# Kernel optimization log

Measured on AMD Instinct MI355X. Metric: run time of the kernel, lower is better.

The kernel has to match this reference:

```python
import jax, jax.numpy as jnp
import numpy as np

MAX_SPAN = 16
EPS = 1e-12


def setup_inputs() -> dict:
    key = jax.random.key(0)
    ks = jax.random.split(key, 10)
    B, S, H, R = 64, 512, 768, 51
    embed = jax.random.normal(ks[0], (B, S, H), dtype=jnp.float32)
    sub_head = jax.random.randint(ks[1], (B,), 0, S - MAX_SPAN, dtype=jnp.int32)
    span = jax.random.randint(ks[2], (B,), 0, MAX_SPAN, dtype=jnp.int32)
    sub_tail = sub_head + span  # guaranteed valid span inside [0, S)
    s = 0.02
    W_ih = jax.random.normal(ks[3], (4 * H, H), dtype=jnp.float32) * s
    W_hh = jax.random.normal(ks[4], (4 * H, H), dtype=jnp.float32) * s
    b_ih = jnp.zeros((4 * H,), dtype=jnp.float32)
    b_hh = jnp.zeros((4 * H,), dtype=jnp.float32)
    cln_weight = jnp.ones((H,), dtype=jnp.float32)
    cln_bias = jnp.zeros((H,), dtype=jnp.float32)
    # nonzero so the conditional path is exercised (init is zeros in torch)
    cln_Ww = jax.random.normal(ks[5], (H, H), dtype=jnp.float32) * s
    cln_Wb = jax.random.normal(ks[6], (H, H), dtype=jnp.float32) * s
    Wh = jax.random.normal(ks[7], (R, H), dtype=jnp.float32) * s
    bh = jnp.zeros((R,), dtype=jnp.float32)
    Wt = jax.random.normal(ks[8], (R, H), dtype=jnp.float32) * s
    bt = jnp.zeros((R,), dtype=jnp.float32)
    return {"embed": embed, "sub_head": sub_head, "sub_tail": sub_tail,
            "W_ih": W_ih, "W_hh": W_hh, "b_ih": b_ih, "b_hh": b_hh,
            "cln_weight": cln_weight, "cln_bias": cln_bias,
            "cln_Ww": cln_Ww, "cln_Wb": cln_Wb,
            "Wh": Wh, "bh": bh, "Wt": Wt, "bt": bt}


def _ragged_lstm(embed, sub_head, sub_tail, W_ih, W_hh, b_ih, b_hh):
    # Pack ragged spans [head, tail] into a padded [B, MAX_SPAN, H] block and
    # run one batched LSTM scan, freezing state once past each span's end.
    B, S, H = embed.shape
    offs = jnp.arange(MAX_SPAN, dtype=sub_head.dtype)
    pos = sub_head[:, None] + offs[None, :]                    # [B, T]
    idx = jnp.clip(pos, 0, S - 1)
    x = jnp.take_along_axis(embed, idx[:, :, None], axis=1)    # [B, T, H]
    mask = pos <= sub_tail[:, None]                            # [B, T]

    def step(carry, inp):
        h, c = carry
        xt, mt = inp                                           # [B,H], [B]
        gates = xt @ W_ih.T + b_ih + h @ W_hh.T + b_hh         # [B, 4H]
        i, f, g, o = jnp.split(gates, 4, axis=-1)
        c_new = jax.nn.sigmoid(f) * c + jax.nn.sigmoid(i) * jnp.tanh(g)
        h_new = jax.nn.sigmoid(o) * jnp.tanh(c_new)
        m = mt[:, None]
        h = jnp.where(m, h_new, h)
        c = jnp.where(m, c_new, c)
        return (h, c), None

    h0 = jnp.zeros((B, H), dtype=embed.dtype)
    (hn, _), _ = jax.lax.scan(step, (h0, h0),
                              (x.transpose(1, 0, 2), mask.T))
    return hn                                                  # [B, H]


def _cond_layernorm(inputs, cond, weight, bias, Ww, Wb):
    # weight/bias are conditioned on `cond` via zero-init dense layers
    w = cond @ Ww.T + weight                                   # [B, H]
    b = cond @ Wb.T + bias
    mu = jnp.mean(inputs, axis=-1, keepdims=True)
    xc = inputs - mu
    var = jnp.mean(xc * xc, axis=-1, keepdims=True)
    std = jnp.sqrt(var + EPS)
    return w[:, None, :] * xc / (std + EPS) + b[:, None, :]


def reference(embed, sub_head, sub_tail, W_ih, W_hh, b_ih, b_hh,
              cln_weight, cln_bias, cln_Ww, cln_Wb, Wh, bh, Wt, bt):
    sub_embed = _ragged_lstm(embed, sub_head, sub_tail, W_ih, W_hh, b_ih, b_hh)
    new_embed = _cond_layernorm(embed, sub_embed, cln_weight, cln_bias,
                                cln_Ww, cln_Wb)
    heads = jax.nn.sigmoid(new_embed @ Wh.T + bh)              # [B, S, R]
    tails = jax.nn.sigmoid(new_embed @ Wt.T + bt)
    return heads, tails
```

## Files before the change

kernel.cpp:

```cpp
#include <hip/hip_runtime.h>

typedef __attribute__((ext_vector_type(8))) short bhalf8;
typedef __attribute__((ext_vector_type(4))) float floatx4;


__device__ unsigned short g_whh[3072*768];
__device__ unsigned short g_wih[3072*768];
__device__ unsigned short g_wcln[1536*768];
__device__ unsigned short g_whl[128*768];
__device__ unsigned short g_h2[2*64*768];
__device__ float g_cbuf[64*768];
__device__ float g_xg[1024*3072];
__device__ float g_wv[64*768], g_bv[64*768];
__device__ float g_bias[3072];
__device__ float g_cw[768], g_cb[768];
__device__ float g_bh[64], g_bt[64];

static __device__ __forceinline__ unsigned short f2bf(float f){
  unsigned u = __builtin_bit_cast(unsigned, f);
  u = (u + 0x7FFFu + ((u >> 16) & 1u)) >> 16;
  return (unsigned short)u;
}
static __device__ __forceinline__ float sigm(float x){ return 1.0f/(1.0f + __expf(-x)); }
static __device__ __forceinline__ float tanhq(float x){ float e = __expf(-2.0f*x); return (1.0f - e)/(1.0f + e); }

__global__ __launch_bounds__(256) void casrel_prep(
    const float* __restrict__ W_ih, const float* __restrict__ W_hh,
    const float* __restrict__ Ww,   const float* __restrict__ Wb,
    const float* __restrict__ Wh,   const float* __restrict__ Wt,
    const float* __restrict__ b_ih, const float* __restrict__ b_hh,
    const float* __restrict__ cw,   const float* __restrict__ cb,
    const float* __restrict__ bh,   const float* __restrict__ bt){
  const long NW = 2359296, NC = 1179648, NL = 98304;
  const long NH = 98304, NCF = 49152, NB = 3072, NV = 768, NR = 64;
  const long total = NW*2 + NC + NL + NH + NCF + NB + NV*2 + NR*2;
  for(long i = (long)blockIdx.x*256 + threadIdx.x; i < total; i += (long)gridDim.x*256){
    long j = i;
    if(j < NW){ g_whh[j] = f2bf(W_hh[j]); continue; } j -= NW;
    if(j < NW){ g_wih[j] = f2bf(W_ih[j]); continue; } j -= NW;
    if(j < NC){ g_wcln[j] = (j < 589824) ? f2bf(Ww[j]) : f2bf(Wb[j - 589824]); continue; } j -= NC;
    if(j < NL){ long r = j / 768, k = j - r*768;
                float v = 0.0f;
                if(r < 51) v = Wh[r*768 + k]; else if(r < 102) v = Wt[(r-51)*768 + k];
                g_whl[j] = f2bf(v); continue; } j -= NL;
    if(j < NH){ g_h2[j] = 0; continue; } j -= NH;
    if(j < NCF){ g_cbuf[j] = 0.0f; continue; } j -= NCF;
    if(j < NB){ g_bias[j] = b_ih[j] + b_hh[j]; continue; } j -= NB;
    if(j < NV){ g_cw[j] = cw[j]; continue; } j -= NV;
    if(j < NV){ g_cb[j] = cb[j]; continue; } j -= NV;
    if(j < NR){ g_bh[j] = (j < 51) ? bh[j] : 0.0f; continue; } j -= NR;
    g_bt[j] = (j < 51) ? bt[j] : 0.0f;
  }
}

__global__ __launch_bounds__(256) void casrel_xgates(
    const float* __restrict__ embed, const int* __restrict__ head){
  __shared__ char sB[128*128];
  const int tid = threadIdx.x, l = tid & 63, w = tid >> 6;
  const int n0 = blockIdx.x * 128;
  const int m0 = blockIdx.y * 64 + w*16;
  const int mrow = m0 + (l & 15);
  const int b = mrow >> 4, t = mrow & 15;
  int pos = head[b] + t; pos = pos < 0 ? 0 : (pos > 511 ? 511 : pos);
  const float* aptr = embed + ((long)b*512 + pos)*768 + ((l >> 4)*8);
  floatx4 acc[8];
  #pragma unroll
  for(int q=0;q<8;q++){ acc[q][0]=0.f; acc[q][1]=0.f; acc[q][2]=0.f; acc[q][3]=0.f; }
  for(int kt=0; kt<12; ++kt){
    __syncthreads();
    #pragma unroll
    for(int j=0;j<4;j++){
      int f = tid + 256*j;
      int row = f >> 3, seg = f & 7;
      uint4 v = *(const uint4*)(g_wih + ((long)(n0+row))*768 + kt*64 + seg*8);
      *(uint4*)(sB + row*128 + ((seg*16) ^ ((row & 7) << 4))) = v;
    }
    __syncthreads();
    #pragma unroll
    for(int ks=0; ks<2; ++ks){
      const int k = kt*64 + ks*32;
      float4 lo = *(const float4*)(aptr + k);
      float4 hi = *(const float4*)(aptr + k + 4);
      bhalf8 a;
      a[0]=(short)f2bf(lo.x); a[1]=(short)f2bf(lo.y); a[2]=(short)f2bf(lo.z); a[3]=(short)f2bf(lo.w);
      a[4]=(short)f2bf(hi.x); a[5]=(short)f2bf(hi.y); a[6]=(short)f2bf(hi.z); a[7]=(short)f2bf(hi.w);
      const int kb = ks*64 + ((l >> 4)*16);
      #pragma unroll
      for(int q=0;q<8;q++){
        int row = q*16 + (l & 15);
        bhalf8 bb = *(const bhalf8*)(sB + row*128 + (kb ^ ((row & 7) << 4)));
        acc[q] = __builtin_amdgcn_mfma_f32_16x16x32_bf16(a, bb, acc[q], 0, 0, 0);
      }
    }
  }
  #pragma unroll
  for(int q=0;q<8;q++){
    const int n = n0 + q*16 + (l & 15);
    const float bias = g_bias[n];
    #pragma unroll
    for(int r=0;r<4;r++){
      const int m = m0 + (l >> 4)*4 + r;
      g_xg[(long)m*3072 + n] = acc[q][r] + bias;
    }
  }
}

__global__ __launch_bounds__(256) void casrel_step(
    const int* __restrict__ head, const int* __restrict__ tail, int t){
  __shared__ char sW[64*768];
  const unsigned short* hin = g_h2 + (t & 1)*49152;
  unsigned short* hout = g_h2 + ((t & 1) ^ 1)*49152;
  const int tid = threadIdx.x, l = tid & 63, w = tid >> 6;
  const int j0 = blockIdx.x * 16;
  const int jown = j0 + (l & 15);
  const int arow = w*16 + (l & 15);
  floatx4 acc[4];
  #pragma unroll
  for(int g=0;g<4;g++){ acc[g][0]=0.f; acc[g][1]=0.f; acc[g][2]=0.f; acc[g][3]=0.f; }
  for(int kt=0; kt<2; ++kt){
    __syncthreads();
    #pragma unroll
    for(int j=0;j<12;j++){
      int f = tid + 256*j;
      int row = f / 48, seg = f - row*48;
      int grow = (row >> 4)*768 + j0 + (row & 15);
      uint4 v = *(const uint4*)(g_whh + (long)grow*768 + kt*384 + seg*8);
      *(uint4*)(sW + row*768 + ((seg*16) ^ ((row & 7) << 4))) = v;
    }
    __syncthreads();
    const unsigned short* ap = hin + arow*768 + kt*384 + ((l >> 4)*8);
    #pragma unroll 4
    for(int ks=0; ks<12; ++ks){
      bhalf8 a = *(const bhalf8*)(ap + ks*32);
      const int kb = ks*64 + ((l >> 4)*16);
      #pragma unroll
      for(int g=0;g<4;g++){
        int row = g*16 + (l & 15);
        bhalf8 bb = *(const bhalf8*)(sW + row*768 + (kb ^ ((row & 7) << 4)));
        acc[g] = __builtin_amdgcn_mfma_f32_16x16x32_bf16(a, bb, acc[g], 0, 0, 0);
      }
    }
  }
  #pragma unroll
  for(int r=0;r<4;r++){
    const int b = w*16 + (l >> 4)*4 + r;
    const int cell = b*768 + jown;
    const float* xp = g_xg + ((long)(b*16 + t))*3072 + jown;
    float Gi = acc[0][r] + xp[0];
    float Gf = acc[1][r] + xp[768];
    float Gg = acc[2][r] + xp[1536];
    float Go = acc[3][r] + xp[2304];
    if(t <= tail[b] - head[b]){
      float c = g_cbuf[cell];
      float ig = sigm(Gi), fg = sigm(Gf), gg = tanhq(Gg), og = sigm(Go);
      c = fg*c + ig*gg;
      g_cbuf[cell] = c;
      hout[cell] = f2bf(og*tanhq(c));
    } else {
      hout[cell] = hin[cell];
    }
  }
}

__global__ __launch_bounds__(256) void casrel_clnproj(){
  __shared__ char sW[32*1536];
  const int tid = threadIdx.x, l = tid & 63, w = tid >> 6;
  const int n0c = blockIdx.x * 32;
  #pragma unroll
  for(int j=0;j<12;j++){
    int f = tid + 256*j;
    int row = f / 96, seg = f - row*96;
    uint4 v = *(const uint4*)(g_wcln + (long)(n0c+row)*768 + seg*8);
    *(uint4*)(sW + row*1536 + ((seg*16) ^ ((row & 7) << 4))) = v;
  }
  __syncthreads();
  const int arow = w*16 + (l & 15);
  floatx4 acc2[2];
  #pragma unroll
  for(int q=0;q<2;q++){ acc2[q][0]=0.f; acc2[q][1]=0.f; acc2[q][2]=0.f; acc2[q][3]=0.f; }
  const unsigned short* ap2 = g_h2 + arow*768 + ((l >> 4)*8);
  for(int ks=0; ks<24; ++ks){
    bhalf8 a = *(const bhalf8*)(ap2 + ks*32);
    const int kb = ks*64 + ((l >> 4)*16);
    #pragma unroll
    for(int q=0;q<2;q++){
      int row = q*16 + (l & 15);
      bhalf8 bb = *(const bhalf8*)(sW + row*1536 + (kb ^ ((row & 7) << 4)));
      acc2[q] = __builtin_amdgcn_mfma_f32_16x16x32_bf16(a, bb, acc2[q], 0, 0, 0);
    }
  }
  #pragma unroll
  for(int q=0;q<2;q++){
    const int n = n0c + q*16 + (l & 15);
    #pragma unroll
    for(int r=0;r<4;r++){
      const int b = w*16 + (l >> 4)*4 + r;
      float v = acc2[q][r];
      if(n < 768) g_wv[b*768 + n] = v + g_cw[n];
      else        g_bv[b*768 + (n - 768)] = v + g_cb[n - 768];
    }
  }
}

__global__ __launch_bounds__(256) void casrel_out(
    const float* __restrict__ embed, float* __restrict__ out){
  __shared__ char sB[128*128];
  __shared__ char sE[32*128];
  __shared__ float sMu[32], sRs[32];
  const int tid = threadIdx.x, l = tid & 63, w = tid >> 6;
  const int b = blockIdx.y;
  const int s0 = blockIdx.x * 32;
  const float* xbase = embed + ((long)b*512 + s0)*768;
  for(int rr=0; rr<8; ++rr){
    const int row = w*8 + rr;
    const float* rp = xbase + row*768;
    float sm = 0.f, sq = 0.f;
    #pragma unroll
    for(int q=0;q<3;q++){
      float4 v = *(const float4*)(rp + l*4 + q*256);
      sm += v.x + v.y + v.z + v.w;
      sq += v.x*v.x + v.y*v.y + v.z*v.z + v.w*v.w;
    }
    #pragma unroll
    for(int o=32;o>0;o>>=1){ sm += __shfl_xor(sm, o); sq += __shfl_xor(sq, o); }
    if(l == 0){
      float mu = sm * (1.0f/768.0f);
      float var = sq * (1.0f/768.0f) - mu*mu;
      sMu[row] = mu;
      sRs[row] = 1.0f/(sqrtf(var + 1e-12f) + 1e-12f);
    }
  }
  __syncthreads();
  const int mf = w >> 1, nb = (w & 1)*4;
  floatx4 acc[4];
  #pragma unroll
  for(int q=0;q<4;q++){ acc[q][0]=0.f; acc[q][1]=0.f; acc[q][2]=0.f; acc[q][3]=0.f; }
  for(int kt=0; kt<12; ++kt){
    __syncthreads();
    #pragma unroll
    for(int j=0;j<4;j++){
      int f = tid + 256*j;
      int row = f >> 3, seg = f & 7;
      uint4 v = *(const uint4*)(g_whl + (long)row*768 + kt*64 + seg*8);
      *(uint4*)(sB + row*128 + ((seg*16) ^ ((row & 7) << 4))) = v;
    }
    #pragma unroll
    for(int j=0;j<2;j++){
      int f = tid + 256*j;
      int row = f >> 4, cs = f & 15;
      int k = kt*64 + cs*4;
      float4 x4 = *(const float4*)(xbase + row*768 + k);
      float4 w4 = *(const float4*)(g_wv + b*768 + k);
      float4 c4 = *(const float4*)(g_bv + b*768 + k);
      float mu = sMu[row], rs = sRs[row];
      unsigned long long pk =
          (unsigned long long)f2bf((x4.x - mu)*rs*w4.x + c4.x)
        | ((unsigned long long)f2bf((x4.y - mu)*rs*w4.y + c4.y) << 16)
        | ((unsigned long long)f2bf((x4.z - mu)*rs*w4.z + c4.z) << 32)
        | ((unsigned long long)f2bf((x4.w - mu)*rs*w4.w + c4.w) << 48);
      *(unsigned long long*)(sE + row*128 + ((cs*8) ^ ((row & 7) << 4))) = pk;
    }
    __syncthreads();
    #pragma unroll
    for(int ks=0; ks<2; ++ks){
      const int arow = mf*16 + (l & 15);
      const int kb = ks*64 + ((l >> 4)*16);
      bhalf8 a = *(const bhalf8*)(sE + arow*128 + (kb ^ ((arow & 7) << 4)));
      #pragma unroll
      for(int q=0;q<4;q++){
        int row = (nb + q)*16 + (l & 15);
        bhalf8 bb = *(const bhalf8*)(sB + row*128 + (kb ^ ((row & 7) << 4)));
        acc[q] = __builtin_amdgcn_mfma_f32_16x16x32_bf16(a, bb, acc[q], 0, 0, 0);
      }
    }
  }
  const long HT = (long)64*512*51;
  #pragma unroll
  for(int q=0;q<4;q++){
    const int n = (nb + q)*16 + (l & 15);
    if(n >= 102) continue;
    const int rr = (n < 51) ? n : (n - 51);
    const long obase = (n < 51) ? 0 : HT;
    const float bias = (n < 51) ? g_bh[n] : g_bt[n - 51];
    #pragma unroll
    for(int r=0;r<4;r++){
      const int s = s0 + mf*16 + (l >> 4)*4 + r;
      out[obase + ((long)b*512 + s)*51 + rr] = sigm(acc[q][r] + bias);
    }
  }
}

extern "C" void kernel_launch(void* const* d_in, const int* in_sizes, int n_in,
                              void* d_out, int out_size, void* d_ws, size_t ws_size,
                              hipStream_t stream){
  const float* embed = (const float*)d_in[0];
  const int*   head  = (const int*)d_in[1];
  const int*   tail  = (const int*)d_in[2];
  const float* W_ih  = (const float*)d_in[3];
  const float* W_hh  = (const float*)d_in[4];
  const float* b_ih  = (const float*)d_in[5];
  const float* b_hh  = (const float*)d_in[6];
  const float* cw    = (const float*)d_in[7];
  const float* cb    = (const float*)d_in[8];
  const float* Ww    = (const float*)d_in[9];
  const float* Wb    = (const float*)d_in[10];
  const float* Wh    = (const float*)d_in[11];
  const float* bh    = (const float*)d_in[12];
  const float* Wt    = (const float*)d_in[13];
  const float* bt    = (const float*)d_in[14];
  float* out = (float*)d_out;
  (void)d_ws; (void)ws_size;

  casrel_prep<<<dim3(4096), dim3(256), 0, stream>>>(W_ih, W_hh, Ww, Wb, Wh, Wt,
                                                    b_ih, b_hh, cw, cb, bh, bt);
  casrel_xgates<<<dim3(24,16), dim3(256), 0, stream>>>(embed, head);
  for(int t=0; t<16; ++t)
    casrel_step<<<dim3(48), dim3(256), 0, stream>>>(head, tail, t);
  casrel_clnproj<<<dim3(48), dim3(256), 0, stream>>>();
  casrel_out<<<dim3(16,64), dim3(256), 0, stream>>>(embed, out);
}
```

Before: 282.2 us.

## Fuse LSTM steps and CLN projection into one cooperative persistent kernel

Replaces the 16 per-timestep LSTM launches and the separate CLN projection launch with one cooperative kernel. It keeps the W_hh slice resident in LDS, holds the cell state in registers and uses grid.sync between steps. It also vectorizes the prep kernel to convert 8 floats per thread. The output kernel now builds bf16 A fragments directly in registers and reads head weights from global memory instead of staging through LDS. This removes launch overhead and repeated weight reloads, but adds grid-wide barriers and unstaged global loads in the output GEMM.

```diff
diff --git a/kernel.cpp b/kernel.cpp
--- a/kernel.cpp
+++ b/kernel.cpp
@@ -1,15 +1,16 @@
 #include <hip/hip_runtime.h>
+#include <hip/hip_cooperative_groups.h>
+
+namespace cg = cooperative_groups;
 
 typedef __attribute__((ext_vector_type(8))) short bhalf8;
 typedef __attribute__((ext_vector_type(4))) float floatx4;
-
 
 __device__ unsigned short g_whh[3072*768];
 __device__ unsigned short g_wih[3072*768];
 __device__ unsigned short g_wcln[1536*768];
 __device__ unsigned short g_whl[128*768];
 __device__ unsigned short g_h2[2*64*768];
-__device__ float g_cbuf[64*768];
 __device__ float g_xg[1024*3072];
 __device__ float g_wv[64*768], g_bv[64*768];
 __device__ float g_bias[3072];
@@ -23,6 +24,17 @@
 }
 static __device__ __forceinline__ float sigm(float x){ return 1.0f/(1.0f + __expf(-x)); }
 static __device__ __forceinline__ float tanhq(float x){ float e = __expf(-2.0f*x); return (1.0f - e)/(1.0f + e); }
+
+static __device__ __forceinline__ void cv8(const float* __restrict__ s, unsigned short* __restrict__ d){
+  float4 a = ((const float4*)s)[0];
+  float4 b = ((const float4*)s)[1];
+  uint4 v;
+  v.x = (unsigned)f2bf(a.x) | ((unsigned)f2bf(a.y) << 16);
+  v.y = (unsigned)f2bf(a.z) | ((unsigned)f2bf(a.w) << 16);
+  v.z = (unsigned)f2bf(b.x) | ((unsigned)f2bf(b.y) << 16);
+  v.w = (unsigned)f2bf(b.z) | ((unsigned)f2bf(b.w) << 16);
+  *(uint4*)d = v;
+}
 
 __global__ __launch_bounds__(256) void casrel_prep(
     const float* __restrict__ W_ih, const float* __restrict__ W_hh,
@@ -31,25 +43,48 @@
     const float* __restrict__ b_ih, const float* __restrict__ b_hh,
     const float* __restrict__ cw,   const float* __restrict__ cb,
     const float* __restrict__ bh,   const float* __restrict__ bt){
-  const long NW = 2359296, NC = 1179648, NL = 98304;
-  const long NH = 98304, NCF = 49152, NB = 3072, NV = 768, NR = 64;
-  const long total = NW*2 + NC + NL + NH + NCF + NB + NV*2 + NR*2;
+  const long CW = 294912;
+  const long CC = 147456;
+  const long CL = 12288;
+  const long CH = 12288;
+  const long CB = 384;
+  const long CV = 96;
+  const long CR = 8;
+  const long total = CW*2 + CC + CL + CH + CB + CV*2 + CR*2;
   for(long i = (long)blockIdx.x*256 + threadIdx.x; i < total; i += (long)gridDim.x*256){
     long j = i;
-    if(j < NW){ g_whh[j] = f2bf(W_hh[j]); continue; } j -= NW;
-    if(j < NW){ g_wih[j] = f2bf(W_ih[j]); continue; } j -= NW;
-    if(j < NC){ g_wcln[j] = (j < 589824) ? f2bf(Ww[j]) : f2bf(Wb[j - 589824]); continue; } j -= NC;
-    if(j < NL){ long r = j / 768, k = j - r*768;
-                float v = 0.0f;
-                if(r < 51) v = Wh[r*768 + k]; else if(r < 102) v = Wt[(r-51)*768 + k];
-                g_whl[j] = f2bf(v); continue; } j -= NL;
-    if(j < NH){ g_h2[j] = 0; continue; } j -= NH;
-    if(j < NCF){ g_cbuf[j] = 0.0f; continue; } j -= NCF;
-    if(j < NB){ g_bias[j] = b_ih[j] + b_hh[j]; continue; } j -= NB;
-    if(j < NV){ g_cw[j] = cw[j]; continue; } j -= NV;
-    if(j < NV){ g_cb[j] = cb[j]; continue; } j -= NV;
-    if(j < NR){ g_bh[j] = (j < 51) ? bh[j] : 0.0f; continue; } j -= NR;
-    g_bt[j] = (j < 51) ? bt[j] : 0.0f;
+    if(j < CW){ cv8(W_hh + j*8, g_whh + j*8); continue; } j -= CW;
+    if(j < CW){ cv8(W_ih + j*8, g_wih + j*8); continue; } j -= CW;
+    if(j < CC){ long e = j*8;
+                if(e < 589824) cv8(Ww + e, g_wcln + e);
+                else           cv8(Wb + (e - 589824), g_wcln + e);
+                continue; } j -= CC;
+    if(j < CL){ long e = j*8;
+                long r = e / 768, k = e - r*768;
+                if(r < 51)       cv8(Wh + r*768 + k, g_whl + e);
+                else if(r < 102) cv8(Wt + (r-51)*768 + k, g_whl + e);
+                else             *(uint4*)(g_whl + e) = make_uint4(0,0,0,0);
+                continue; } j -= CL;
+    if(j < CH){ *(uint4*)(g_h2 + j*8) = make_uint4(0,0,0,0); continue; } j -= CH;
+    if(j < CB){ long e = j*8;
+                #pragma unroll
+                for(int q=0;q<8;q++) g_bias[e+q] = b_ih[e+q] + b_hh[e+q];
+                continue; } j -= CB;
+    if(j < CV){ long e = j*8;
+                *(float4*)(g_cw + e)     = *(const float4*)(cw + e);
+                *(float4*)(g_cw + e + 4) = *(const float4*)(cw + e + 4);
+                continue; } j -= CV;
+    if(j < CV){ long e = j*8;
+                *(float4*)(g_cb + e)     = *(const float4*)(cb + e);
+                *(float4*)(g_cb + e + 4) = *(const float4*)(cb + e + 4);
+                continue; } j -= CV;
+    if(j < CR){ long e = j*8;
+                #pragma unroll
+                for(int q=0;q<8;q++){ long n = e+q; g_bh[n] = (n < 51) ? bh[n] : 0.0f; }
+                continue; } j -= CR;
+    { long e = j*8;
+      #pragma unroll
+      for(int q=0;q<8;q++){ long n = e+q; g_bt[n] = (n < 51) ? bt[n] : 0.0f; } }
   }
 }
 
@@ -105,68 +140,73 @@
   }
 }
 
-__global__ __launch_bounds__(256) void casrel_step(
-    const int* __restrict__ head, const int* __restrict__ tail, int t){
-  __shared__ char sW[64*768];
-  const unsigned short* hin = g_h2 + (t & 1)*49152;
-  unsigned short* hout = g_h2 + ((t & 1) ^ 1)*49152;
+__global__ __launch_bounds__(256) void casrel_lstm(
+    const int* __restrict__ head, const int* __restrict__ tail){
+  __shared__ char sW[64*1536];
+  cg::grid_group grid = cg::this_grid();
   const int tid = threadIdx.x, l = tid & 63, w = tid >> 6;
   const int j0 = blockIdx.x * 16;
+  #pragma unroll 4
+  for(int j=0;j<24;j++){
+    int f = tid + 256*j;
+    int row = f / 96, seg = f - row*96;
+    int grow = (row >> 4)*768 + j0 + (row & 15);
+    uint4 v = *(const uint4*)(g_whh + (long)grow*768 + seg*8);
+    *(uint4*)(sW + row*1536 + ((seg*16) ^ ((row & 7) << 4))) = v;
+  }
+  __syncthreads();
+  float creg[4];
+  int spown[4];
+  #pragma unroll
+  for(int r=0;r<4;r++){
+    int b = w*16 + (l >> 4)*4 + r;
+    spown[r] = tail[b] - head[b];
+    creg[r] = 0.f;
+  }
   const int jown = j0 + (l & 15);
   const int arow = w*16 + (l & 15);
-  floatx4 acc[4];
-  #pragma unroll
-  for(int g=0;g<4;g++){ acc[g][0]=0.f; acc[g][1]=0.f; acc[g][2]=0.f; acc[g][3]=0.f; }
-  for(int kt=0; kt<2; ++kt){
-    __syncthreads();
-    #pragma unroll
-    for(int j=0;j<12;j++){
-      int f = tid + 256*j;
-      int row = f / 48, seg = f - row*48;
-      int grow = (row >> 4)*768 + j0 + (row & 15);
-      uint4 v = *(const uint4*)(g_whh + (long)grow*768 + kt*384 + seg*8);
-      *(uint4*)(sW + row*768 + ((seg*16) ^ ((row & 7) << 4))) = v;
-    }
-    __syncthreads();
-    const unsigned short* ap = hin + arow*768 + kt*384 + ((l >> 4)*8);
-    #pragma unroll 4
-    for(int ks=0; ks<12; ++ks){
+  for(int t=0;t<16;t++){
+    const unsigned short* hin = g_h2 + (t & 1)*49152;
+    unsigned short* hout = g_h2 + ((t & 1) ^ 1)*49152;
+    floatx4 acc[4];
+    #pragma unroll
+    for(int g=0;g<4;g++){ acc[g][0]=0.f; acc[g][1]=0.f; acc[g][2]=0.f; acc[g][3]=0.f; }
+    const unsigned short* ap = hin + arow*768 + ((l >> 4)*8);
+    #pragma unroll 6
+    for(int ks=0; ks<24; ++ks){
       bhalf8 a = *(const bhalf8*)(ap + ks*32);
       const int kb = ks*64 + ((l >> 4)*16);
       #pragma unroll
       for(int g=0;g<4;g++){
         int row = g*16 + (l & 15);
-        bhalf8 bb = *(const bhalf8*)(sW + row*768 + (kb ^ ((row & 7) << 4)));
+        bhalf8 bb = *(const bhalf8*)(sW + row*1536 + (kb ^ ((row & 7) << 4)));
         acc[g] = __builtin_amdgcn_mfma_f32_16x16x32_bf16(a, bb, acc[g], 0, 0, 0);
       }
     }
-  }
-  #pragma unroll
-  for(int r=0;r<4;r++){
-    const int b = w*16 + (l >> 4)*4 + r;
-    const int cell = b*768 + jown;
-    const float* xp = g_xg + ((long)(b*16 + t))*3072 + jown;
-    float Gi = acc[0][r] + xp[0];
-    float Gf = acc[1][r] + xp[768];
-    float Gg = acc[2][r] + xp[1536];
-    float Go = acc[3][r] + xp[2304];
-    if(t <= tail[b] - head[b]){
-      float c = g_cbuf[cell];
-      float ig = sigm(Gi), fg = sigm(Gf), gg = tanhq(Gg), og = sigm(Go);
-      c = fg*c + ig*gg;
-      g_cbuf[cell] = c;
-      hout[cell] = f2bf(og*tanhq(c));
-    } else {
-      hout[cell] = hin[cell];
-    }
-  }
-}
-
-__global__ __launch_bounds__(256) void casrel_clnproj(){
-  __shared__ char sW[32*1536];
-  const int tid = threadIdx.x, l = tid & 63, w = tid >> 6;
+    #pragma unroll
+    for(int r=0;r<4;r++){
+      const int b = w*16 + (l >> 4)*4 + r;
+      const float* xp = g_xg + ((long)(b*16 + t))*3072 + jown;
+      float Gi = acc[0][r] + xp[0];
+      float Gf = acc[1][r] + xp[768];
+      float Gg = acc[2][r] + xp[1536];
+      float Go = acc[3][r] + xp[2304];
+      unsigned short hv;
+      if(t <= spown[r]){
+        float ig = sigm(Gi), fg = sigm(Gf), gg = tanhq(Gg), og = sigm(Go);
+        creg[r] = fg*creg[r] + ig*gg;
+        hv = f2bf(og*tanhq(creg[r]));
+      } else {
+        hv = hin[b*768 + jown];
+      }
+      hout[b*768 + jown] = hv;
+    }
+    __threadfence();
+    grid.sync();
+  }
+  __syncthreads();
   const int n0c = blockIdx.x * 32;
-  #pragma unroll
+  #pragma unroll 4
   for(int j=0;j<12;j++){
     int f = tid + 256*j;
     int row = f / 96, seg = f - row*96;
@@ -174,7 +214,6 @@
     *(uint4*)(sW + row*1536 + ((seg*16) ^ ((row & 7) << 4))) = v;
   }
   __syncthreads();
-  const int arow = w*16 + (l & 15);
   floatx4 acc2[2];
   #pragma unroll
   for(int q=0;q<2;q++){ acc2[q][0]=0.f; acc2[q][1]=0.f; acc2[q][2]=0.f; acc2[q][3]=0.f; }
@@ -204,8 +243,6 @@
 
 __global__ __launch_bounds__(256) void casrel_out(
     const float* __restrict__ embed, float* __restrict__ out){
-  __shared__ char sB[128*128];
-  __shared__ char sE[32*128];
   __shared__ float sMu[32], sRs[32];
   const int tid = threadIdx.x, l = tid & 63, w = tid >> 6;
   const int b = blockIdx.y;
@@ -232,46 +269,36 @@
   }
   __syncthreads();
   const int mf = w >> 1, nb = (w & 1)*4;
+  const int lrow = mf*16 + (l & 15);
+  const float mu = sMu[lrow], rs = sRs[lrow];
+  const float* aeb = embed + ((long)b*512 + s0 + lrow)*768;
+  const float* wvb = g_wv + b*768;
+  const float* bvb = g_bv + b*768;
   floatx4 acc[4];
   #pragma unroll
   for(int q=0;q<4;q++){ acc[q][0]=0.f; acc[q][1]=0.f; acc[q][2]=0.f; acc[q][3]=0.f; }
-  for(int kt=0; kt<12; ++kt){
-    __syncthreads();
-    #pragma unroll
-    for(int j=0;j<4;j++){
-      int f = tid + 256*j;
-      int row = f >> 3, seg = f & 7;
-      uint4 v = *(const uint4*)(g_whl + (long)row*768 + kt*64 + seg*8);
-      *(uint4*)(sB + row*128 + ((seg*16) ^ ((row & 7) << 4))) = v;
-    }
-    #pragma unroll
-    for(int j=0;j<2;j++){
-      int f = tid + 256*j;
-      int row = f >> 4, cs = f & 15;
-      int k = kt*64 + cs*4;
-      float4 x4 = *(const float4*)(xbase + row*768 + k);
-      float4 w4 = *(const float4*)(g_wv + b*768 + k);
-      float4 c4 = *(const float4*)(g_bv + b*768 + k);
-      float mu = sMu[row], rs = sRs[row];
-      unsigned long long pk =
-          (unsigned long long)f2bf((x4.x - mu)*rs*w4.x + c4.x)
-        | ((unsigned long long)f2bf((x4.y - mu)*rs*w4.y + c4.y) << 16)
-        | ((unsigned long long)f2bf((x4.z - mu)*rs*w4.z + c4.z) << 32)
-        | ((unsigned long long)f2bf((x4.w - mu)*rs*w4.w + c4.w) << 48);
-      *(unsigned long long*)(sE + row*128 + ((cs*8) ^ ((row & 7) << 4))) = pk;
-    }
-    __syncthreads();
-    #pragma unroll
-    for(int ks=0; ks<2; ++ks){
-      const int arow = mf*16 + (l & 15);
-      const int kb = ks*64 + ((l >> 4)*16);
-      bhalf8 a = *(const bhalf8*)(sE + arow*128 + (kb ^ ((arow & 7) << 4)));
-      #pragma unroll
-      for(int q=0;q<4;q++){
-        int row = (nb + q)*16 + (l & 15);
-        bhalf8 bb = *(const bhalf8*)(sB + row*128 + (kb ^ ((row & 7) << 4)));
-        acc[q] = __builtin_amdgcn_mfma_f32_16x16x32_bf16(a, bb, acc[q], 0, 0, 0);
-      }
+  for(int ks=0; ks<24; ++ks){
+    const int k = ks*32 + ((l >> 4)*8);
+    float4 xlo = *(const float4*)(aeb + k);
+    float4 xhi = *(const float4*)(aeb + k + 4);
+    float4 wlo = *(const float4*)(wvb + k);
+    float4 whi = *(const float4*)(wvb + k + 4);
+    float4 clo = *(const float4*)(bvb + k);
+    float4 chi = *(const float4*)(bvb + k + 4);
+    bhalf8 a;
+    a[0]=(short)f2bf((xlo.x - mu)*rs*wlo.x + clo.x);
+    a[1]=(short)f2bf((xlo.y - mu)*rs*wlo.y + clo.y);
+    a[2]=(short)f2bf((xlo.z - mu)*rs*wlo.z + clo.z);
+    a[3]=(short)f2bf((xlo.w - mu)*rs*wlo.w + clo.w);
+    a[4]=(short)f2bf((xhi.x - mu)*rs*whi.x + chi.x);
+    a[5]=(short)f2bf((xhi.y - mu)*rs*whi.y + chi.y);
+    a[6]=(short)f2bf((xhi.z - mu)*rs*whi.z + chi.z);
+    a[7]=(short)f2bf((xhi.w - mu)*rs*whi.w + chi.w);
+    #pragma unroll
+    for(int q=0;q<4;q++){
+      const int row = (nb + q)*16 + (l & 15);
+      bhalf8 bb = *(const bhalf8*)(g_whl + (long)row*768 + k);
+      acc[q] = __builtin_amdgcn_mfma_f32_16x16x32_bf16(a, bb, acc[q], 0, 0, 0);
     }
   }
   const long HT = (long)64*512*51;
@@ -311,11 +338,12 @@
   float* out = (float*)d_out;
   (void)d_ws; (void)ws_size;
 
-  casrel_prep<<<dim3(4096), dim3(256), 0, stream>>>(W_ih, W_hh, Ww, Wb, Wh, Wt,
+  casrel_prep<<<dim3(2048), dim3(256), 0, stream>>>(W_ih, W_hh, Ww, Wb, Wh, Wt,
                                                     b_ih, b_hh, cw, cb, bh, bt);
   casrel_xgates<<<dim3(24,16), dim3(256), 0, stream>>>(embed, head);
-  for(int t=0; t<16; ++t)
-    casrel_step<<<dim3(48), dim3(256), 0, stream>>>(head, tail, t);
-  casrel_clnproj<<<dim3(48), dim3(256), 0, stream>>>();
+  {
+    void* args[] = {(void*)&head, (void*)&tail};
+    hipLaunchCooperativeKernel((void*)casrel_lstm, dim3(48), dim3(256), args, 0, stream);
+  }
   casrel_out<<<dim3(16,64), dim3(256), 0, stream>>>(embed, out);
 }
```

Measured after the change: 481.9 us. 1.71x slower.
